# Performance work log

Measured on AMD Instinct MI355X. Metric: run time of the kernel, lower is better.

The kernel has to match this reference:

```python
import jax, jax.numpy as jnp
import numpy as np

NUM_ITERATIONS = 3
NUM_SLOTS = 8
SLOT_SIZE = 256
MLP_HIDDEN = 512
EPSILON = 1e-8
LN_EPS = 1e-5


def _ln(x, w, b):
    m = jnp.mean(x, axis=-1, keepdims=True)
    v = jnp.var(x, axis=-1, keepdims=True)
    return (x - m) * jax.lax.rsqrt(v + LN_EPS) * w + b


def _gru_cell(x, h, w_ih, w_hh, b_ih, b_hh):
    # torch.nn.GRUCell semantics; gates ordered [r, z, n]
    gi = x @ w_ih.T + b_ih
    gh = h @ w_hh.T + b_hh
    ir, iz, inn = jnp.split(gi, 3, axis=-1)
    hr, hz, hn = jnp.split(gh, 3, axis=-1)
    r = jax.nn.sigmoid(ir + hr)
    z = jax.nn.sigmoid(iz + hz)
    n = jnp.tanh(inn + r * hn)
    return (1.0 - z) * n + z * h


def setup_inputs() -> dict:
    key = jax.random.key(0)
    ks = jax.random.split(key, 12)
    D, H = SLOT_SIZE, MLP_HIDDEN
    s = 0.02
    return {
        "inputs": jax.random.normal(ks[0], (64, 4096, D), dtype=jnp.float32),
        "noise": jax.random.normal(ks[1], (64, NUM_SLOTS, D), dtype=jnp.float32),
        "ln_in_w": jnp.ones((D,), jnp.float32), "ln_in_b": jnp.zeros((D,), jnp.float32),
        "ln_slots_w": jnp.ones((D,), jnp.float32), "ln_slots_b": jnp.zeros((D,), jnp.float32),
        "ln_mlp_w": jnp.ones((D,), jnp.float32), "ln_mlp_b": jnp.zeros((D,), jnp.float32),
        "slots_mu": jax.random.normal(ks[2], (1, 1, D), jnp.float32) * s,
        "slots_log_sigma": jnp.zeros((1, 1, D), jnp.float32),
        "Wq": jax.random.normal(ks[3], (D, D), jnp.float32) * s,
        "Wk": jax.random.normal(ks[4], (D, D), jnp.float32) * s,
        "Wv": jax.random.normal(ks[5], (D, D), jnp.float32) * s,
        "gru_w_ih": jax.random.normal(ks[6], (3 * D, D), jnp.float32) * s,
        "gru_w_hh": jax.random.normal(ks[7], (3 * D, D), jnp.float32) * s,
        "gru_b_ih": jnp.zeros((3 * D,), jnp.float32),
        "gru_b_hh": jnp.zeros((3 * D,), jnp.float32),
        "mlp_w1": jax.random.normal(ks[8], (H, D), jnp.float32) * s,
        "mlp_b1": jnp.zeros((H,), jnp.float32),
        "mlp_w2": jax.random.normal(ks[9], (D, H), jnp.float32) * s,
        "mlp_b2": jnp.zeros((D,), jnp.float32),
    }


def reference(inputs, noise, ln_in_w, ln_in_b, ln_slots_w, ln_slots_b, ln_mlp_w, ln_mlp_b,
              slots_mu, slots_log_sigma, Wq, Wk, Wv,
              gru_w_ih, gru_w_hh, gru_b_ih, gru_b_hh,
              mlp_w1, mlp_b1, mlp_w2, mlp_b2):
    B, N, D = inputs.shape
    S = NUM_SLOTS
    x = _ln(inputs, ln_in_w, ln_in_b)            # [B,N,D]
    k = x @ Wk.T                                  # [B,N,D]
    v = x @ Wv.T                                  # [B,N,D]
    slots = slots_mu + jnp.exp(slots_log_sigma) * noise   # [B,S,D]
    scale = D ** (-0.5)
    for _ in range(NUM_ITERATIONS):
        slots_prev = slots
        s_n = _ln(slots, ln_slots_w, ln_slots_b)
        q = (s_n @ Wq.T) * scale                  # [B,S,D]
        attn_logits = jnp.einsum('bnd,bsd->bns', k, q)
        attn = jax.nn.softmax(attn_logits, axis=-1) + EPSILON
        attn = attn / jnp.sum(attn, axis=-2, keepdims=True)   # renorm over inputs
        updates = jnp.einsum('bns,bnd->bsd', attn, v)          # [B,S,D]
        slots = _gru_cell(updates.reshape(-1, D), slots_prev.reshape(-1, D),
                          gru_w_ih, gru_w_hh, gru_b_ih, gru_b_hh).reshape(B, S, D)
        h = jax.nn.relu(_ln(slots, ln_mlp_w, ln_mlp_b) @ mlp_w1.T + mlp_b1)
        slots = slots + (h @ mlp_w2.T + mlp_b2)
    return slots
```

## Files before the change

kernel.cpp:

```cpp
#include <hip/hip_runtime.h>

#define CB 64
#define CN 4096
#define CD 256
#define CS 8
#define CH 512

typedef __bf16 bf16_t;
typedef bf16_t bf16x8 __attribute__((ext_vector_type(8)));
typedef float f32x4 __attribute__((ext_vector_type(4)));

__device__ __forceinline__ unsigned short f2bf(float f){
  unsigned int u = __builtin_bit_cast(unsigned int, f);
  u += 0x7FFFu + ((u >> 16) & 1u);
  return (unsigned short)(u >> 16);
}

__device__ __forceinline__ f32x4 mfma16(bf16x8 a, bf16x8 b, f32x4 c){
  return __builtin_amdgcn_mfma_f32_16x16x32_bf16(a, b, c, 0, 0, 0);
}

__device__ __forceinline__ void gl_lds16(const void* g, void* l){
  __builtin_amdgcn_global_load_lds(
      (const __attribute__((address_space(1))) unsigned int*)g,
      (__attribute__((address_space(3))) unsigned int*)l, 16, 0, 0);
}

__global__ __launch_bounds__(256) void k_ln(const float* __restrict__ in,
    const float* __restrict__ gw, const float* __restrict__ gb,
    unsigned short* __restrict__ x){
  int blk = blockIdx.x;
  int b = blk >> 6, nt = blk & 63;
  int wv = threadIdx.x >> 6, l = threadIdx.x & 63;
  const float* base = in + ((size_t)b*CN + (size_t)nt*64) * CD;
  unsigned short* xb = x + ((size_t)b*CN + (size_t)nt*64) * CD;
  float4 w4 = *(const float4*)(gw + 4*l);
  float4 b4 = *(const float4*)(gb + 4*l);
  for(int i = 0; i < 16; i++){
    int r = wv*16 + i;
    float4 v = *(const float4*)(base + (size_t)r*CD + 4*l);
    float s1 = v.x + v.y + v.z + v.w;
    float s2 = v.x*v.x + v.y*v.y + v.z*v.z + v.w*v.w;
    #pragma unroll
    for(int m = 1; m < 64; m <<= 1){ s1 += __shfl_xor(s1, m); s2 += __shfl_xor(s2, m); }
    float mean = s1 * (1.0f/CD);
    float var  = fmaxf(s2 * (1.0f/CD) - mean*mean, 0.0f);
    float rstd = rsqrtf(var + 1e-5f);
    float y0 = (v.x - mean)*rstd*w4.x + b4.x;
    float y1 = (v.y - mean)*rstd*w4.y + b4.y;
    float y2 = (v.z - mean)*rstd*w4.z + b4.z;
    float y3 = (v.w - mean)*rstd*w4.w + b4.w;
    uint2 p;
    p.x = (unsigned)f2bf(y0) | ((unsigned)f2bf(y1) << 16);
    p.y = (unsigned)f2bf(y2) | ((unsigned)f2bf(y3) << 16);
    *(uint2*)(xb + (size_t)r*CD + 4*l) = p;
  }
}

__global__ __launch_bounds__(256) void k_slots0(const float* __restrict__ noise,
    const float* __restrict__ mu, const float* __restrict__ lsig, float* __restrict__ slots){
  int i = blockIdx.x*256 + threadIdx.x;
  int d = i & 255;
  slots[i] = mu[d] + __expf(lsig[d]) * noise[i];
}

__global__ __launch_bounds__(256) void k_m1t(const float* __restrict__ Wq,
    const float* __restrict__ Wk, unsigned short* __restrict__ M1T){
  int ep = blockIdx.x, e = threadIdx.x;
  float acc = 0.0f;
  for(int d = 0; d < 256; d++) acc = fmaf(Wq[(size_t)d*256 + e], Wk[(size_t)d*256 + ep], acc);
  M1T[(size_t)ep*256 + e] = f2bf(acc * 0.0625f);
}

__global__ __launch_bounds__(256) void k_miht(const float* __restrict__ wih,
    const float* __restrict__ Wv, float* __restrict__ MihT){
  int j = blockIdx.x, e = threadIdx.x;
  float acc = 0.0f;
  for(int d = 0; d < 256; d++) acc = fmaf(wih[(size_t)j*256 + d], Wv[(size_t)d*256 + e], acc);
  MihT[(size_t)e*768 + j] = acc;
}

__global__ void k_tr(const float* __restrict__ src, float* __restrict__ dst){
  int r = blockIdx.x, c = threadIdx.x;
  int R = gridDim.x, C = blockDim.x;
  dst[(size_t)c*R + r] = src[(size_t)r*C + c];
}

__global__ __launch_bounds__(256) void k_qt(const float* __restrict__ slots,
    const float* __restrict__ lw, const float* __restrict__ lb,
    const unsigned short* __restrict__ M1T, unsigned short* __restrict__ qt){
  __shared__ unsigned short sn[16*264];
  int b = blockIdx.x;
  int wv = threadIdx.x >> 6, l = threadIdx.x & 63;
  int lm = l & 15, lg = l >> 4;
  float4 w4 = *(const float4*)(lw + 4*l);
  float4 b4 = *(const float4*)(lb + 4*l);
  for(int i = 0; i < 2; i++){
    int r = wv*2 + i;
    float4 v = *(const float4*)(slots + ((size_t)b*CS + r)*CD + 4*l);
    float s1 = v.x + v.y + v.z + v.w;
    float s2 = v.x*v.x + v.y*v.y + v.z*v.z + v.w*v.w;
    #pragma unroll
    for(int m = 1; m < 64; m <<= 1){ s1 += __shfl_xor(s1, m); s2 += __shfl_xor(s2, m); }
    float mean = s1 * (1.0f/CD);
    float var  = fmaxf(s2 * (1.0f/CD) - mean*mean, 0.0f);
    float rstd = rsqrtf(var + 1e-5f);
    float y0 = (v.x - mean)*rstd*w4.x + b4.x;
    float y1 = (v.y - mean)*rstd*w4.y + b4.y;
    float y2 = (v.z - mean)*rstd*w4.z + b4.z;
    float y3 = (v.w - mean)*rstd*w4.w + b4.w;
    uint2 p;
    p.x = (unsigned)f2bf(y0) | ((unsigned)f2bf(y1) << 16);
    p.y = (unsigned)f2bf(y2) | ((unsigned)f2bf(y3) << 16);
    *(uint2*)(&sn[r*264 + 4*l]) = p;
    uint2 z; z.x = 0u; z.y = 0u;
    *(uint2*)(&sn[(r+8)*264 + 4*l]) = z;
  }
  __syncthreads();
  bf16x8 af[8];
  #pragma unroll
  for(int k = 0; k < 8; k++) af[k] = *(const bf16x8*)(&sn[lm*264 + k*32 + lg*8]);
  #pragma unroll
  for(int ntile = 0; ntile < 4; ntile++){
    int ep = wv*64 + ntile*16 + lm;
    f32x4 acc = {0.f, 0.f, 0.f, 0.f};
    const unsigned short* mrow = M1T + (size_t)ep*CD;
    #pragma unroll
    for(int k = 0; k < 8; k++){
      bf16x8 bf = *(const bf16x8*)(mrow + k*32 + lg*8);
      acc = mfma16(af[k], bf, acc);
    }
    #pragma unroll
    for(int reg = 0; reg < 4; reg++){
      int s = lg*4 + reg;
      qt[((size_t)b*16 + s)*CD + ep] = f2bf(acc[reg]);
    }
  }
}

__global__ __launch_bounds__(256) void k_attn(const unsigned short* __restrict__ x,
    const unsigned short* __restrict__ qt, float* __restrict__ U, float* __restrict__ den){
  __shared__ unsigned short xt[64*256];
  __shared__ unsigned short pt[16*72];
  int b = blockIdx.x >> 3, chunk = blockIdx.x & 7;
  int wv = threadIdx.x >> 6, l = threadIdx.x & 63;
  int lm = l & 15, lg = l >> 4;

  bf16x8 qb[8];
  const unsigned short* qrow = qt + ((size_t)b*16 + lm)*CD;
  #pragma unroll
  for(int k = 0; k < 8; k++) qb[k] = *(const bf16x8*)(qrow + k*32 + lg*8);

  f32x4 uacc[4];
  #pragma unroll
  for(int nt = 0; nt < 4; nt++){ f32x4 z = {0.f,0.f,0.f,0.f}; uacc[nt] = z; }
  float dacc = 0.0f;

  const unsigned short* xbatch = x + (size_t)b*CN*CD + (size_t)chunk*512*CD;

  for(int t = 0; t < 8; t++){
    const unsigned short* xtile = xbatch + (size_t)t*64*CD;
    __syncthreads();
    #pragma unroll
    for(int k2 = 0; k2 < 8; k2++){
      int r0 = wv*16 + k2*2;
      int row = r0 + (l >> 5);
      int c = l & 31;
      int f = (row >> 3) & 3;
      const unsigned short* g = xtile + (size_t)row*CD + (size_t)(c ^ f)*8;
      gl_lds16(g, &xt[r0*CD]);
    }
    __syncthreads();

    f32x4 c4 = {0.f, 0.f, 0.f, 0.f};
    int rowl = wv*16 + lm;
    int f1 = (rowl >> 3) & 3;
    #pragma unroll
    for(int k = 0; k < 8; k++){
      int cc = (k*4 + lg) ^ f1;
      bf16x8 a = *(const bf16x8*)(&xt[rowl*256 + cc*8]);
      c4 = mfma16(a, qb[k], c4);
    }
    float pv[4];
    #pragma unroll
    for(int reg = 0; reg < 4; reg++){
      float v = (lm < 8) ? c4[reg] : -1e30f;
      float mx = v;
      #pragma unroll
      for(int m = 1; m < 16; m <<= 1) mx = fmaxf(mx, __shfl_xor(mx, m));
      float e = __expf(v - mx);
      float s = e;
      #pragma unroll
      for(int m = 1; m < 16; m <<= 1) s += __shfl_xor(s, m);
      float p = (lm < 8) ? (e/s + 1e-8f) : 0.0f;
      dacc += p;
      pv[reg] = p;
    }
    int rbase = wv*16 + lg*4;
    unsigned int p01 = (unsigned)f2bf(pv[0]) | ((unsigned)f2bf(pv[1]) << 16);
    unsigned int p23 = (unsigned)f2bf(pv[2]) | ((unsigned)f2bf(pv[3]) << 16);
    *(unsigned int*)(&pt[lm*72 + rbase])     = p01;
    *(unsigned int*)(&pt[lm*72 + rbase + 2]) = p23;
    __syncthreads();

    #pragma unroll
    for(int ks = 0; ks < 2; ks++){
      bf16x8 a = *(const bf16x8*)(&pt[lm*72 + ks*32 + lg*8]);
      int rb = ks*32 + lg*8;
      int f2 = (rb >> 3) & 3;
      #pragma unroll
      for(int nt = 0; nt < 4; nt++){
        int e = wv*64 + nt*16 + lm;
        int cidx = ((e >> 3) ^ f2);
        bf16x8 bfr;
        #pragma unroll
        for(int j = 0; j < 8; j++){
          unsigned short tv = xt[(rb + j)*256 + cidx*8 + (e & 7)];
          bfr[j] = __builtin_bit_cast(bf16_t, tv);
        }
        uacc[nt] = mfma16(a, bfr, uacc[nt]);
      }
    }
  }

  dacc += __shfl_xor(dacc, 16);
  dacc += __shfl_xor(dacc, 32);
  if(l < 8) atomicAdd(&den[b*CS + l], dacc);
  if(lg < 2){
    #pragma unroll
    for(int nt = 0; nt < 4; nt++){
      #pragma unroll
      for(int reg = 0; reg < 4; reg++){
        int s = lg*4 + reg;
        atomicAdd(&U[((size_t)b*CS + s)*CD + wv*64 + nt*16 + lm], uacc[nt][reg]);
      }
    }
  }
}

template<int MT, int TM, int EPI>
__global__ __launch_bounds__(256) void k_gemm(
    const float* __restrict__ A, int lda, const float* __restrict__ B, int ldb,
    float* __restrict__ C, int ldc, int K, int ntn,
    const float* __restrict__ bias, const float* __restrict__ res,
    const float* __restrict__ A2, const float* __restrict__ B2, float* __restrict__ C2){
  __shared__ float AsT[32*(MT+1)];
  __shared__ float Bs[32*68];
  if(blockIdx.y == 1){ A = A2; B = B2; C = C2; }
  int bm = blockIdx.x / ntn, bn = blockIdx.x % ntn;
  int m0 = bm*MT, n0 = bn*64;
  int tid = threadIdx.x;
  int tx = tid & 15, ty = tid >> 4;
  float acc[TM][4];
  #pragma unroll
  for(int i = 0; i < TM; i++)
    #pragma unroll
    for(int j = 0; j < 4; j++) acc[i][j] = 0.0f;

  for(int k0 = 0; k0 < K; k0 += 32){
    __syncthreads();
    #pragma unroll
    for(int v = 0; v < MT/32; v++){
      int idx = v*256 + tid;
      int ar = idx >> 3, ac = (idx & 7)*4;
      float4 a4 = *(const float4*)(A + (size_t)(m0+ar)*lda + k0 + ac);
      AsT[(ac+0)*(MT+1) + ar] = a4.x;
      AsT[(ac+1)*(MT+1) + ar] = a4.y;
      AsT[(ac+2)*(MT+1) + ar] = a4.z;
      AsT[(ac+3)*(MT+1) + ar] = a4.w;
    }
    #pragma unroll
    for(int v = 0; v < 2; v++){
      int idx = v*256 + tid;
      int kr = idx >> 4, c4 = (idx & 15)*4;
      *(float4*)(&Bs[kr*68 + c4]) = *(const float4*)(B + (size_t)(k0+kr)*ldb + n0 + c4);
    }
    __syncthreads();
    #pragma unroll
    for(int k = 0; k < 32; k++){
      float av[TM];
      #pragma unroll
      for(int i = 0; i < TM; i++) av[i] = AsT[k*(MT+1) + ty*TM + i];
      float4 bv = *(const float4*)(&Bs[k*68 + tx*4]);
      #pragma unroll
      for(int i = 0; i < TM; i++){
        acc[i][0] = fmaf(av[i], bv.x, acc[i][0]);
        acc[i][1] = fmaf(av[i], bv.y, acc[i][1]);
        acc[i][2] = fmaf(av[i], bv.z, acc[i][2]);
        acc[i][3] = fmaf(av[i], bv.w, acc[i][3]);
      }
    }
  }
  int n = n0 + tx*4;
  float4 bi;
  if(EPI != 0) bi = *(const float4*)(bias + n);
  #pragma unroll
  for(int i = 0; i < TM; i++){
    int m = m0 + ty*TM + i;
    float4 o;
    if(EPI == 0){
      o.x = acc[i][0]; o.y = acc[i][1]; o.z = acc[i][2]; o.w = acc[i][3];
    } else if(EPI == 1){
      o.x = fmaxf(acc[i][0] + bi.x, 0.0f);
      o.y = fmaxf(acc[i][1] + bi.y, 0.0f);
      o.z = fmaxf(acc[i][2] + bi.z, 0.0f);
      o.w = fmaxf(acc[i][3] + bi.w, 0.0f);
    } else {
      float4 rv = *(const float4*)(res + (size_t)m*ldc + n);
      o.x = acc[i][0] + bi.x + rv.x;
      o.y = acc[i][1] + bi.y + rv.y;
      o.z = acc[i][2] + bi.z + rv.z;
      o.w = acc[i][3] + bi.w + rv.w;
    }
    *(float4*)(C + (size_t)m*ldc + n) = o;
  }
}

__global__ __launch_bounds__(256) void k_act(const float* __restrict__ gi,
    const float* __restrict__ gh, const float* __restrict__ den,
    const float* __restrict__ slots, const float* __restrict__ bih,
    const float* __restrict__ bhh, const float* __restrict__ lw,
    const float* __restrict__ lb, float* __restrict__ hp, float* __restrict__ lnh){
  int wv = threadIdx.x >> 6, l = threadIdx.x & 63;
  int row = blockIdx.x*4 + wv;
  const float* gir = gi + (size_t)row*768;
  const float* ghr = gh + (size_t)row*768;
  float invd = 1.0f / den[row];
  float4 air = *(const float4*)(gir + 4*l);
  float4 aiz = *(const float4*)(gir + 256 + 4*l);
  float4 ain = *(const float4*)(gir + 512 + 4*l);
  float4 ahr = *(const float4*)(ghr + 4*l);
  float4 ahz = *(const float4*)(ghr + 256 + 4*l);
  float4 ahn = *(const float4*)(ghr + 512 + 4*l);
  float4 br = *(const float4*)(bih + 4*l);
  float4 bz = *(const float4*)(bih + 256 + 4*l);
  float4 bn = *(const float4*)(bih + 512 + 4*l);
  float4 cr = *(const float4*)(bhh + 4*l);
  float4 cz = *(const float4*)(bhh + 256 + 4*l);
  float4 cn = *(const float4*)(bhh + 512 + 4*l);
  float4 hc = *(const float4*)(slots + (size_t)row*256 + 4*l);
  float4 h;
  #pragma unroll
  for(int i = 0; i < 4; i++){
    float gr = (&air.x)[i]*invd + (&br.x)[i] + (&ahr.x)[i] + (&cr.x)[i];
    float gz = (&aiz.x)[i]*invd + (&bz.x)[i] + (&ahz.x)[i] + (&cz.x)[i];
    float gn = (&ain.x)[i]*invd + (&bn.x)[i];
    float hn = (&ahn.x)[i] + (&cn.x)[i];
    float r = 1.0f/(1.0f + __expf(-gr));
    float z = 1.0f/(1.0f + __expf(-gz));
    float n = tanhf(gn + r*hn);
    (&h.x)[i] = (1.0f - z)*n + z*(&hc.x)[i];
  }
  *(float4*)(hp + (size_t)row*256 + 4*l) = h;
  float s1 = h.x + h.y + h.z + h.w;
  float s2 = h.x*h.x + h.y*h.y + h.z*h.z + h.w*h.w;
  #pragma unroll
  for(int m = 1; m < 64; m <<= 1){ s1 += __shfl_xor(s1, m); s2 += __shfl_xor(s2, m); }
  float mean = s1 * (1.0f/CD);
  float var  = fmaxf(s2 * (1.0f/CD) - mean*mean, 0.0f);
  float rstd = rsqrtf(var + 1e-5f);
  float4 w4 = *(const float4*)(lw + 4*l);
  float4 b4 = *(const float4*)(lb + 4*l);
  float4 o;
  o.x = (h.x - mean)*rstd*w4.x + b4.x;
  o.y = (h.y - mean)*rstd*w4.y + b4.y;
  o.z = (h.z - mean)*rstd*w4.z + b4.z;
  o.w = (h.w - mean)*rstd*w4.w + b4.w;
  *(float4*)(lnh + (size_t)row*256 + 4*l) = o;
}

extern "C" void kernel_launch(void* const* d_in, const int* in_sizes, int n_in,
                              void* d_out, int out_size, void* d_ws, size_t ws_size,
                              hipStream_t stream){
  const float* inputs = (const float*)d_in[0];
  const float* noise  = (const float*)d_in[1];
  const float* ln_in_w = (const float*)d_in[2];
  const float* ln_in_b = (const float*)d_in[3];
  const float* ln_sl_w = (const float*)d_in[4];
  const float* ln_sl_b = (const float*)d_in[5];
  const float* ln_ml_w = (const float*)d_in[6];
  const float* ln_ml_b = (const float*)d_in[7];
  const float* mu   = (const float*)d_in[8];
  const float* lsig = (const float*)d_in[9];
  const float* Wq  = (const float*)d_in[10];
  const float* Wk  = (const float*)d_in[11];
  const float* Wv  = (const float*)d_in[12];
  const float* wih = (const float*)d_in[13];
  const float* whh = (const float*)d_in[14];
  const float* bih = (const float*)d_in[15];
  const float* bhh = (const float*)d_in[16];
  const float* w1  = (const float*)d_in[17];
  const float* b1  = (const float*)d_in[18];
  const float* w2  = (const float*)d_in[19];
  const float* b2  = (const float*)d_in[20];

  char* ws = (char*)d_ws;
  size_t off = 0;
  unsigned short* x = (unsigned short*)(ws + off); off += (size_t)CB*CN*CD*2;
  float* slots = (float*)(ws + off); off += (size_t)CB*CS*CD*4;
  float* hp    = (float*)(ws + off); off += (size_t)CB*CS*CD*4;
  float* U     = (float*)(ws + off); off += (size_t)CB*CS*CD*4;
  float* den   = (float*)(ws + off); off += (size_t)CB*CS*4;
  unsigned short* qt  = (unsigned short*)(ws + off); off += (size_t)CB*16*CD*2;
  unsigned short* M1T = (unsigned short*)(ws + off); off += (size_t)CD*CD*2;
  float* MihT = (float*)(ws + off); off += (size_t)CD*768*4;
  float* WhhT = (float*)(ws + off); off += (size_t)CD*768*4;
  float* w1T  = (float*)(ws + off); off += (size_t)CD*CH*4;
  float* w2T  = (float*)(ws + off); off += (size_t)CH*CD*4;
  float* gi   = (float*)(ws + off); off += (size_t)512*768*4;
  float* gh   = (float*)(ws + off); off += (size_t)512*768*4;
  float* lnh  = (float*)(ws + off); off += (size_t)512*256*4;
  float* h1   = (float*)(ws + off); off += (size_t)512*512*4;

  k_ln<<<4096, 256, 0, stream>>>(inputs, ln_in_w, ln_in_b, x);
  k_slots0<<<512, 256, 0, stream>>>(noise, mu, lsig, slots);
  k_m1t<<<256, 256, 0, stream>>>(Wq, Wk, M1T);
  k_miht<<<768, 256, 0, stream>>>(wih, Wv, MihT);
  k_tr<<<768, 256, 0, stream>>>(whh, WhhT);
  k_tr<<<512, 256, 0, stream>>>(w1, w1T);
  k_tr<<<256, 512, 0, stream>>>(w2, w2T);

  for(int it = 0; it < 3; it++){
    k_qt<<<64, 256, 0, stream>>>(slots, ln_sl_w, ln_sl_b, M1T, qt);
    hipMemsetAsync(U, 0, ((size_t)CB*CS*CD + (size_t)CB*CS)*4, stream);
    k_attn<<<512, 256, 0, stream>>>(x, qt, U, den);
    k_gemm<64, 4, 0><<<dim3(96, 2), 256, 0, stream>>>(
        U, 256, MihT, 768, gi, 768, 256, 12, nullptr, nullptr,
        slots, WhhT, gh);
    k_act<<<128, 256, 0, stream>>>(gi, gh, den, slots, bih, bhh, ln_ml_w, ln_ml_b, hp, lnh);
    k_gemm<64, 4, 1><<<dim3(64, 1), 256, 0, stream>>>(
        lnh, 256, w1T, 512, h1, 512, 256, 8, b1, nullptr,
        nullptr, nullptr, nullptr);
    k_gemm<32, 2, 2><<<dim3(64, 1), 256, 0, stream>>>(
        h1, 512, w2T, 256, slots, 256, 512, 4, b2, hp,
        nullptr, nullptr, nullptr);
  }
  hipMemcpyAsync(d_out, slots, (size_t)CB*CS*CD*4, hipMemcpyDeviceToDevice, stream);
}
```

Measured before the change: 826.7 us.

## Merge setup kernels, fold memset into k_qt, split attention finer, widen swizzle

Six setup launches are merged into one k_setup kernel with block-range dispatch. The per-iteration memset of U/den moves into k_qt, and the final memcpy is dropped by having the last GEMM write straight to the output. The attention kernel doubles its grid to 1024 blocks, each handling 256 tokens instead of 512, to raise occupancy. The LDS swizzle is widened to an 8-way XOR pattern to cut bank conflicts. In exchange, the finer split doubles the atomicAdd traffic into U.

```diff
diff --git a/kernel.cpp b/kernel.cpp
--- a/kernel.cpp
+++ b/kernel.cpp
@@ -57,41 +57,57 @@
   }
 }
 
-__global__ __launch_bounds__(256) void k_slots0(const float* __restrict__ noise,
-    const float* __restrict__ mu, const float* __restrict__ lsig, float* __restrict__ slots){
-  int i = blockIdx.x*256 + threadIdx.x;
-  int d = i & 255;
-  slots[i] = mu[d] + __expf(lsig[d]) * noise[i];
-}
-
-__global__ __launch_bounds__(256) void k_m1t(const float* __restrict__ Wq,
-    const float* __restrict__ Wk, unsigned short* __restrict__ M1T){
-  int ep = blockIdx.x, e = threadIdx.x;
-  float acc = 0.0f;
-  for(int d = 0; d < 256; d++) acc = fmaf(Wq[(size_t)d*256 + e], Wk[(size_t)d*256 + ep], acc);
-  M1T[(size_t)ep*256 + e] = f2bf(acc * 0.0625f);
-}
-
-__global__ __launch_bounds__(256) void k_miht(const float* __restrict__ wih,
-    const float* __restrict__ Wv, float* __restrict__ MihT){
-  int j = blockIdx.x, e = threadIdx.x;
-  float acc = 0.0f;
-  for(int d = 0; d < 256; d++) acc = fmaf(wih[(size_t)j*256 + d], Wv[(size_t)d*256 + e], acc);
-  MihT[(size_t)e*768 + j] = acc;
-}
-
-__global__ void k_tr(const float* __restrict__ src, float* __restrict__ dst){
-  int r = blockIdx.x, c = threadIdx.x;
-  int R = gridDim.x, C = blockDim.x;
-  dst[(size_t)c*R + r] = src[(size_t)r*C + c];
+__global__ __launch_bounds__(256) void k_setup(
+    const float* __restrict__ Wq, const float* __restrict__ Wk,
+    const float* __restrict__ wih, const float* __restrict__ Wv,
+    const float* __restrict__ whh, const float* __restrict__ w1,
+    const float* __restrict__ w2, const float* __restrict__ noise,
+    const float* __restrict__ mu, const float* __restrict__ lsig,
+    unsigned short* __restrict__ M1T, float* __restrict__ MihT,
+    float* __restrict__ WhhT, float* __restrict__ w1T,
+    float* __restrict__ w2T, float* __restrict__ slots){
+  int bid = blockIdx.x, tid = threadIdx.x;
+  if(bid < 256){
+    int ep = bid, e = tid;
+    float acc = 0.0f;
+    for(int d = 0; d < 256; d++) acc = fmaf(Wq[(size_t)d*256 + e], Wk[(size_t)d*256 + ep], acc);
+    M1T[(size_t)ep*256 + e] = f2bf(acc * 0.0625f);
+  } else if(bid < 1024){
+    int j = bid - 256, e = tid;
+    float acc = 0.0f;
+    for(int d = 0; d < 256; d++) acc = fmaf(wih[(size_t)j*256 + d], Wv[(size_t)d*256 + e], acc);
+    MihT[(size_t)e*768 + j] = acc;
+  } else if(bid < 1792){
+    int r = bid - 1024, c = tid;
+    WhhT[(size_t)c*768 + r] = whh[(size_t)r*256 + c];
+  } else if(bid < 2304){
+    int r = bid - 1792, c = tid;
+    w1T[(size_t)c*512 + r] = w1[(size_t)r*256 + c];
+  } else if(bid < 2816){
+    int idx = (bid - 2304)*256 + tid;
+    int r = idx >> 9, c = idx & 511;
+    w2T[(size_t)c*256 + r] = w2[(size_t)r*512 + c];
+  } else {
+    int idx = (bid - 2816)*256 + tid;
+    int d = idx & 255;
+    slots[idx] = mu[d] + __expf(lsig[d]) * noise[idx];
+  }
 }
 
 __global__ __launch_bounds__(256) void k_qt(const float* __restrict__ slots,
     const float* __restrict__ lw, const float* __restrict__ lb,
-    const unsigned short* __restrict__ M1T, unsigned short* __restrict__ qt){
+    const unsigned short* __restrict__ M1T, unsigned short* __restrict__ qt,
+    float* __restrict__ U, float* __restrict__ den){
   __shared__ unsigned short sn[16*264];
   int b = blockIdx.x;
-  int wv = threadIdx.x >> 6, l = threadIdx.x & 63;
+  int tid = threadIdx.x;
+  float4 z4 = {0.f, 0.f, 0.f, 0.f};
+  float* Ub = U + (size_t)b*CS*CD;
+  *(float4*)(Ub + tid*8)     = z4;
+  *(float4*)(Ub + tid*8 + 4) = z4;
+  if(tid < CS) den[b*CS + tid] = 0.0f;
+
+  int wv = tid >> 6, l = tid & 63;
   int lm = l & 15, lg = l >> 4;
   float4 w4 = *(const float4*)(lw + 4*l);
   float4 b4 = *(const float4*)(lb + 4*l);
@@ -113,8 +129,8 @@
     p.x = (unsigned)f2bf(y0) | ((unsigned)f2bf(y1) << 16);
     p.y = (unsigned)f2bf(y2) | ((unsigned)f2bf(y3) << 16);
     *(uint2*)(&sn[r*264 + 4*l]) = p;
-    uint2 z; z.x = 0u; z.y = 0u;
-    *(uint2*)(&sn[(r+8)*264 + 4*l]) = z;
+    uint2 zz; zz.x = 0u; zz.y = 0u;
+    *(uint2*)(&sn[(r+8)*264 + 4*l]) = zz;
   }
   __syncthreads();
   bf16x8 af[8];
@@ -142,7 +158,7 @@
     const unsigned short* __restrict__ qt, float* __restrict__ U, float* __restrict__ den){
   __shared__ unsigned short xt[64*256];
   __shared__ unsigned short pt[16*72];
-  int b = blockIdx.x >> 3, chunk = blockIdx.x & 7;
+  int b = blockIdx.x >> 4, chunk = blockIdx.x & 15;
   int wv = threadIdx.x >> 6, l = threadIdx.x & 63;
   int lm = l & 15, lg = l >> 4;
 
@@ -156,9 +172,9 @@
   for(int nt = 0; nt < 4; nt++){ f32x4 z = {0.f,0.f,0.f,0.f}; uacc[nt] = z; }
   float dacc = 0.0f;
 
-  const unsigned short* xbatch = x + (size_t)b*CN*CD + (size_t)chunk*512*CD;
-
-  for(int t = 0; t < 8; t++){
+  const unsigned short* xbatch = x + (size_t)b*CN*CD + (size_t)chunk*256*CD;
+
+  for(int t = 0; t < 4; t++){
     const unsigned short* xtile = xbatch + (size_t)t*64*CD;
     __syncthreads();
     #pragma unroll
@@ -166,7 +182,7 @@
       int r0 = wv*16 + k2*2;
       int row = r0 + (l >> 5);
       int c = l & 31;
-      int f = (row >> 3) & 3;
+      int f = (row ^ (row >> 3)) & 7;
       const unsigned short* g = xtile + (size_t)row*CD + (size_t)(c ^ f)*8;
       gl_lds16(g, &xt[r0*CD]);
     }
@@ -174,7 +190,7 @@
 
     f32x4 c4 = {0.f, 0.f, 0.f, 0.f};
     int rowl = wv*16 + lm;
-    int f1 = (rowl >> 3) & 3;
+    int f1 = (rowl ^ (rowl >> 3)) & 7;
     #pragma unroll
     for(int k = 0; k < 8; k++){
       int cc = (k*4 + lg) ^ f1;
@@ -207,15 +223,16 @@
     for(int ks = 0; ks < 2; ks++){
       bf16x8 a = *(const bf16x8*)(&pt[lm*72 + ks*32 + lg*8]);
       int rb = ks*32 + lg*8;
-      int f2 = (rb >> 3) & 3;
       #pragma unroll
       for(int nt = 0; nt < 4; nt++){
         int e = wv*64 + nt*16 + lm;
-        int cidx = ((e >> 3) ^ f2);
         bf16x8 bfr;
         #pragma unroll
         for(int j = 0; j < 8; j++){
-          unsigned short tv = xt[(rb + j)*256 + cidx*8 + (e & 7)];
+          int row2 = rb + j;
+          int f2 = (row2 ^ (row2 >> 3)) & 7;
+          int cidx = (e >> 3) ^ f2;
+          unsigned short tv = xt[row2*256 + cidx*8 + (e & 7)];
           bfr[j] = __builtin_bit_cast(bf16_t, tv);
         }
         uacc[nt] = mfma16(a, bfr, uacc[nt]);
@@ -413,17 +430,12 @@
   float* h1   = (float*)(ws + off); off += (size_t)512*512*4;
 
   k_ln<<<4096, 256, 0, stream>>>(inputs, ln_in_w, ln_in_b, x);
-  k_slots0<<<512, 256, 0, stream>>>(noise, mu, lsig, slots);
-  k_m1t<<<256, 256, 0, stream>>>(Wq, Wk, M1T);
-  k_miht<<<768, 256, 0, stream>>>(wih, Wv, MihT);
-  k_tr<<<768, 256, 0, stream>>>(whh, WhhT);
-  k_tr<<<512, 256, 0, stream>>>(w1, w1T);
-  k_tr<<<256, 512, 0, stream>>>(w2, w2T);
+  k_setup<<<3328, 256, 0, stream>>>(Wq, Wk, wih, Wv, whh, w1, w2, noise, mu, lsig,
+                                    M1T, MihT, WhhT, w1T, w2T, slots);
 
   for(int it = 0; it < 3; it++){
-    k_qt<<<64, 256, 0, stream>>>(slots, ln_sl_w, ln_sl_b, M1T, qt);
-    hipMemsetAsync(U, 0, ((size_t)CB*CS*CD + (size_t)CB*CS)*4, stream);
-    k_attn<<<512, 256, 0, stream>>>(x, qt, U, den);
+    k_qt<<<64, 256, 0, stream>>>(slots, ln_sl_w, ln_sl_b, M1T, qt, U, den);
+    k_attn<<<1024, 256, 0, stream>>>(x, qt, U, den);
     k_gemm<64, 4, 0><<<dim3(96, 2), 256, 0, stream>>>(
         U, 256, MihT, 768, gi, 768, 256, 12, nullptr, nullptr,
         slots, WhhT, gh);
@@ -431,9 +443,9 @@
     k_gemm<64, 4, 1><<<dim3(64, 1), 256, 0, stream>>>(
         lnh, 256, w1T, 512, h1, 512, 256, 8, b1, nullptr,
         nullptr, nullptr, nullptr);
+    float* cdst = (it == 2) ? (float*)d_out : slots;
     k_gemm<32, 2, 2><<<dim3(64, 1), 256, 0, stream>>>(
-        h1, 512, w2T, 256, slots, 256, 512, 4, b2, hp,
+        h1, 512, w2T, 256, cdst, 256, 512, 4, b2, hp,
         nullptr, nullptr, nullptr);
   }
-  hipMemcpyAsync(d_out, slots, (size_t)CB*CS*CD*4, hipMemcpyDeviceToDevice, stream);
-}
+}
```

Result: faster. 805.0 us (-2.6%).
